# Kernel tuning notes

Hardware: AMD Instinct MI355X
Metric: run time of the kernel (lower is better)

## Reference

```python
import jax, jax.numpy as jnp
import numpy as np

DEPTH = 8
N_FEATURES = 512
N_CLASSES = 1000
N_LEAVES = 2 ** DEPTH          # 256
N_INTERNAL = N_LEAVES - 1      # 255
BATCH = 16384


def _path_tables():
    """Static routing tables for a complete binary tree (heap indexing).

    nodes[d, l] = internal node index visited at level d on the path to leaf l
    bits[d, l]  = 1 if path goes right at that node, else 0
    """
    leaves = np.arange(N_LEAVES)
    nodes = np.stack([(2 ** d - 1) + (leaves >> (DEPTH - d)) for d in range(DEPTH)])
    bits = np.stack([(leaves >> (DEPTH - 1 - d)) & 1 for d in range(DEPTH)])
    return nodes, bits


_NODES, _BITS = _path_tables()


def setup_inputs() -> dict:
    key = jax.random.key(0)
    k1, k2, k3 = jax.random.split(key, 3)
    x = jax.random.normal(k1, (BATCH, N_FEATURES), dtype=jnp.float32)
    # xavier-uniform-ish scale for the stacked gate weights
    gate_w = jax.random.normal(k2, (N_INTERNAL, N_FEATURES), dtype=jnp.float32) / np.sqrt(N_FEATURES)
    gate_b = jnp.zeros((N_INTERNAL,), dtype=jnp.float32)
    leaf_logits = jax.random.normal(k3, (N_LEAVES, N_CLASSES), dtype=jnp.float32) * 0.1
    return {"x": x, "gate_w": gate_w, "gate_b": gate_b, "leaf_logits": leaf_logits}


def reference(x, gate_w, gate_b, leaf_logits):
    # All internal-node gates as one batched matmul: [B, N_INTERNAL]
    p_right = jax.nn.sigmoid(jnp.einsum("bf,nf->bn", x, gate_w) + gate_b)
    # Arrival probability of each leaf: product of branch probs along its path.
    mu = jnp.ones((x.shape[0], N_LEAVES), dtype=x.dtype)
    for d in range(DEPTH):  # static loop over tree depth (8 iters)
        g = p_right[:, _NODES[d]]                       # [B, N_LEAVES]
        branch = jnp.where(_BITS[d] == 1, g, 1.0 - g)   # right vs left prob
        mu = mu * branch
    # Leaf class distributions: softmax per leaf over classes
    leaf_dists = jax.nn.softmax(leaf_logits, axis=-1)   # [N_LEAVES, N_CLASSES]
    return mu @ leaf_dists                              # [B, N_CLASSES]
```

## Files before the change

### kernel.cpp

```cpp
#include <hip/hip_runtime.h>

typedef __attribute__((ext_vector_type(8))) _Float16 f16x8;
typedef __attribute__((ext_vector_type(4))) _Float16 f16x4;
typedef __attribute__((ext_vector_type(4))) float   f32x4;

#define BATCH 16384
#define NFEAT 512
#define NCLS  1000
#define NLEAF 256
#define NINT  255
#define LDP   72
#define PSTR  257

__global__ __launch_bounds__(256) void prep(const float* __restrict__ L,
                                            _Float16* __restrict__ distF,
                                            const float* __restrict__ gw,
                                            _Float16* __restrict__ gwF) {
  const int t = threadIdx.x;
  const int wave = t >> 6, lane = t & 63;
  if (blockIdx.x >= 256) {
    const int p = (blockIdx.x - 256) * 4 + wave;
    const int c = (p >> 4) * 16 + (lane & 15);
    const int k0 = (p & 15) * 32 + (lane >> 4) * 8;
    f16x8 o = {};
    if (c < NINT) {
      float4 v0 = *(const float4*)&gw[(size_t)c * NFEAT + k0];
      float4 v1 = *(const float4*)&gw[(size_t)c * NFEAT + k0 + 4];
      o[0] = (_Float16)v0.x; o[1] = (_Float16)v0.y;
      o[2] = (_Float16)v0.z; o[3] = (_Float16)v0.w;
      o[4] = (_Float16)v1.x; o[5] = (_Float16)v1.y;
      o[6] = (_Float16)v1.z; o[7] = (_Float16)v1.w;
    }
    *(f16x8*)&gwF[((size_t)p * 64 + lane) * 8] = o;
    return;
  }
  __shared__ float red[4];
  const int l = blockIdx.x;
  const int kt = l >> 5, lhi_l = (l >> 3) & 3, jj = l & 7;
  float v[4];
  const bool live = t < 250;
  if (live) {
    float4 f = *(const float4*)&L[(size_t)l * NCLS + t * 4];
    v[0] = f.x; v[1] = f.y; v[2] = f.z; v[3] = f.w;
  } else {
    v[0] = v[1] = v[2] = v[3] = -1e30f;
  }
  float mx = fmaxf(fmaxf(v[0], v[1]), fmaxf(v[2], v[3]));
#pragma unroll
  for (int s = 32; s; s >>= 1) mx = fmaxf(mx, __shfl_xor(mx, s));
  if (lane == 0) red[wave] = mx;
  __syncthreads();
  mx = fmaxf(fmaxf(red[0], red[1]), fmaxf(red[2], red[3]));
  __syncthreads();
  float e[4], sum = 0.f;
#pragma unroll
  for (int i = 0; i < 4; ++i) { e[i] = __expf(v[i] - mx); sum += e[i]; }
  if (!live) { e[0] = e[1] = e[2] = e[3] = 0.f; sum = 0.f; }
#pragma unroll
  for (int s = 32; s; s >>= 1) sum += __shfl_xor(sum, s);
  if (lane == 0) red[wave] = sum;
  __syncthreads();
  sum = red[0] + red[1] + red[2] + red[3];
  float inv = 1.f / sum;
#pragma unroll
  for (int i = 0; i < 4; ++i) {
    int c = t * 4 + i;
    float val = live ? e[i] * inv : 0.f;
    int c16 = c >> 4, ln = c & 15;
    size_t idx = (((size_t)(c16 * 8 + kt)) * 64 + lhi_l * 16 + ln) * 8 + jj;
    distF[idx] = (_Float16)val;
  }
}

__global__ __launch_bounds__(1024)
void g1mu(const float* __restrict__ x, const _Float16* __restrict__ gwF,
          const float* __restrict__ gb, _Float16* __restrict__ muFg) {
  __shared__ union {
    _Float16 A[64 * LDP];
    float P[64 * PSTR];
  } sm;

  const int tid  = threadIdx.x;
  const int wave = tid >> 6, lane = tid & 63;
  const int ln15 = lane & 15, lhi = lane >> 4;
  const int r0 = blockIdx.x * 64;

  f32x4 acc1[4] = {};
  const int arow = tid >> 4, acol = (tid & 15) * 4;

  float4 pa = *(const float4*)&x[(size_t)(r0 + arow) * NFEAT + acol];
  for (int k = 0; k < NFEAT / 64; ++k) {
    {
      f16x4 h;
      h[0] = (_Float16)pa.x; h[1] = (_Float16)pa.y;
      h[2] = (_Float16)pa.z; h[3] = (_Float16)pa.w;
      *(f16x4*)&sm.A[arow * LDP + acol] = h;
    }
    __syncthreads();
    if (k < NFEAT / 64 - 1)
      pa = *(const float4*)&x[(size_t)(r0 + arow) * NFEAT + (k + 1) * 64 + acol];
#pragma unroll
    for (int kk = 0; kk < 2; ++kk) {
      f16x8 a[4];
#pragma unroll
      for (int m = 0; m < 4; ++m)
        a[m] = *(const f16x8*)&sm.A[(m * 16 + ln15) * LDP + kk * 32 + lhi * 8];
      f16x8 b = *(const f16x8*)&gwF[(((size_t)wave * 16 + k * 2 + kk) * 64 + lane) * 8];
#pragma unroll
      for (int m = 0; m < 4; ++m)
        acc1[m] = __builtin_amdgcn_mfma_f32_16x16x32_f16(a[m], b, acc1[m], 0, 0, 0);
    }
    __syncthreads();
  }

  {
    int col = wave * 16 + ln15;
    float bb = (col < NINT) ? gb[col] : 0.f;
#pragma unroll
    for (int m = 0; m < 4; ++m)
#pragma unroll
      for (int j = 0; j < 4; ++j) {
        int rl = m * 16 + lhi * 4 + j;
        float v = acc1[m][j] + bb;
        sm.P[rl * PSTR + col] = 1.f / (1.f + __expf(-v));
      }
  }
  __syncthreads();

  const int lf   = lane * 4;
  const int g_hi = lane >> 3;
  const int sub  = ((lane >> 1) & 3) * 16;
  const int j4   = (lane & 1) * 4;
#pragma unroll
  for (int rr = 0; rr < 4; ++rr) {
    int row = wave * 4 + rr;
    const float* p = &sm.P[row * PSTR];
    float pre = 1.f;
#pragma unroll
    for (int d = 0; d < 6; ++d) {
      int node = (1 << d) - 1 + (lf >> (8 - d));
      int bit  = (lf >> (7 - d)) & 1;
      float g = p[node];
      pre *= bit ? g : (1.f - g);
    }
    float g6  = p[63 + lane];
    float g7a = p[127 + 2 * lane];
    float g7b = p[128 + 2 * lane];
    f16x4 o;
    o[0] = (_Float16)(pre * (1.f - g6) * (1.f - g7a));
    o[1] = (_Float16)(pre * (1.f - g6) * g7a);
    o[2] = (_Float16)(pre * g6 * (1.f - g7b));
    o[3] = (_Float16)(pre * g6 * g7b);
    int row_g = r0 + row;
    size_t idx = (((size_t)(row_g >> 4) * 8 + g_hi) * 64 + sub + (row_g & 15)) * 8 + j4;
    *(f16x4*)&muFg[idx] = o;
  }
}

__global__ __launch_bounds__(256)
void g2(const _Float16* __restrict__ muFg, const _Float16* __restrict__ distF,
        float* __restrict__ out) {
  __shared__ _Float16 sMu[4 * 8 * 64 * 8];
  const int tid  = threadIdx.x;
  const int wave = tid >> 6, lane = tid & 63;
  const int ln15 = lane & 15, lhi = lane >> 4;
  const int bx = blockIdx.x;
  const int by = blockIdx.y;

  {
    const f16x8* src = (const f16x8*)(muFg + (size_t)bx * 16384);
    f16x8* dst = (f16x8*)sMu;
#pragma unroll
    for (int i = 0; i < 8; ++i)
      dst[tid + i * 256] = src[tid + i * 256];
  }
  __syncthreads();

  for (int h = 0; h < 4; ++h) {
    const int c16 = by * 16 + wave * 4 + h;
    f16x8 bb[8];
#pragma unroll
    for (int kk = 0; kk < 8; ++kk)
      bb[kk] = *(const f16x8*)&distF[(((size_t)c16 * 8 + kk) * 64 + lane) * 8];
#pragma unroll
    for (int g = 0; g < 4; ++g) {
      f32x4 acc = {};
#pragma unroll
      for (int kk = 0; kk < 8; ++kk) {
        f16x8 aa = *(const f16x8*)&sMu[((g * 8 + kk) * 64 + lane) * 8];
        acc = __builtin_amdgcn_mfma_f32_16x16x32_f16(bb[kk], aa, acc, 0, 0, 0);
      }
      const int brow = (bx * 4 + g) * 16 + ln15;
      const int col4 = c16 * 16 + lhi * 4;
      if (col4 < NCLS)
        *(f32x4*)&out[(size_t)brow * NCLS + col4] = acc;
    }
  }
}

extern "C" void kernel_launch(void* const* d_in, const int* in_sizes, int n_in,
                              void* d_out, int out_size, void* d_ws, size_t ws_size,
                              hipStream_t stream) {
  const float* x  = (const float*)d_in[0];
  const float* gw = (const float*)d_in[1];
  const float* gb = (const float*)d_in[2];
  const float* ll = (const float*)d_in[3];
  float* out = (float*)d_out;
  char* ws = (char*)d_ws;

  _Float16* gwF   = (_Float16*)(ws);
  _Float16* distF = (_Float16*)(ws + 262144);
  _Float16* muFg  = (_Float16*)(ws + 786432);

  prep <<<320, 256, 0, stream>>>(ll, distF, gw, gwF);
  g1mu <<<BATCH / 64, 1024, 0, stream>>>(x, gwF, gb, muFg);
  g2   <<<dim3(BATCH / 64, 4), 256, 0, stream>>>(muFg, distF, out);
}
```

Measured before the change: 53.79 us.

## Fuse gate/mu kernel with leaf-distribution GEMM, keeping mu in LDS

Merges the g1mu and g2 kernels into one 1024-thread kernel per 64-row block. The mu tile now stays in shared memory instead of going out to and back from a global workspace, and one kernel launch is removed. With 16 waves per block, each wave covers 4 column groups, so all 1000 classes are handled in one block instead of being split across 4 y-blocks. The cost is fewer blocks (256) doing the second GEMM and higher LDS use per block, which may reduce parallelism on the output phase.

New measurement: 101.5 us. 88.6% more time.

```diff
diff --git a/kernel.cpp b/kernel.cpp
--- a/kernel.cpp
+++ b/kernel.cpp
@@ -73,12 +73,14 @@
 }
 
 __global__ __launch_bounds__(1024)
-void g1mu(const float* __restrict__ x, const _Float16* __restrict__ gwF,
-          const float* __restrict__ gb, _Float16* __restrict__ muFg) {
+void fused(const float* __restrict__ x, const _Float16* __restrict__ gwF,
+           const float* __restrict__ gb, const _Float16* __restrict__ distF,
+           float* __restrict__ out) {
   __shared__ union {
     _Float16 A[64 * LDP];
     float P[64 * PSTR];
   } sm;
+  __shared__ _Float16 sMu[4 * 8 * 64 * 8];
 
   const int tid  = threadIdx.x;
   const int wave = tid >> 6, lane = tid & 63;
@@ -151,33 +153,13 @@
     o[1] = (_Float16)(pre * (1.f - g6) * g7a);
     o[2] = (_Float16)(pre * g6 * (1.f - g7b));
     o[3] = (_Float16)(pre * g6 * g7b);
-    int row_g = r0 + row;
-    size_t idx = (((size_t)(row_g >> 4) * 8 + g_hi) * 64 + sub + (row_g & 15)) * 8 + j4;
-    *(f16x4*)&muFg[idx] = o;
-  }
-}
-
-__global__ __launch_bounds__(256)
-void g2(const _Float16* __restrict__ muFg, const _Float16* __restrict__ distF,
-        float* __restrict__ out) {
-  __shared__ _Float16 sMu[4 * 8 * 64 * 8];
-  const int tid  = threadIdx.x;
-  const int wave = tid >> 6, lane = tid & 63;
-  const int ln15 = lane & 15, lhi = lane >> 4;
-  const int bx = blockIdx.x;
-  const int by = blockIdx.y;
-
-  {
-    const f16x8* src = (const f16x8*)(muFg + (size_t)bx * 16384);
-    f16x8* dst = (f16x8*)sMu;
-#pragma unroll
-    for (int i = 0; i < 8; ++i)
-      dst[tid + i * 256] = src[tid + i * 256];
+    size_t idx = (((size_t)(row >> 4) * 8 + g_hi) * 64 + sub + (row & 15)) * 8 + j4;
+    *(f16x4*)&sMu[idx] = o;
   }
   __syncthreads();
 
   for (int h = 0; h < 4; ++h) {
-    const int c16 = by * 16 + wave * 4 + h;
+    const int c16 = wave * 4 + h;
     f16x8 bb[8];
 #pragma unroll
     for (int kk = 0; kk < 8; ++kk)
@@ -190,7 +172,7 @@
         f16x8 aa = *(const f16x8*)&sMu[((g * 8 + kk) * 64 + lane) * 8];
         acc = __builtin_amdgcn_mfma_f32_16x16x32_f16(bb[kk], aa, acc, 0, 0, 0);
       }
-      const int brow = (bx * 4 + g) * 16 + ln15;
+      const int brow = r0 + g * 16 + ln15;
       const int col4 = c16 * 16 + lhi * 4;
       if (col4 < NCLS)
         *(f32x4*)&out[(size_t)brow * NCLS + col4] = acc;
@@ -210,9 +192,7 @@
 
   _Float16* gwF   = (_Float16*)(ws);
   _Float16* distF = (_Float16*)(ws + 262144);
-  _Float16* muFg  = (_Float16*)(ws + 786432);
 
-  prep <<<320, 256, 0, stream>>>(ll, distF, gw, gwF);
-  g1mu <<<BATCH / 64, 1024, 0, stream>>>(x, gwF, gb, muFg);
-  g2   <<<dim3(BATCH / 64, 4), 256, 0, stream>>>(muFg, distF, out);
+  prep  <<<320, 256, 0, stream>>>(ll, distF, gw, gwF);
+  fused <<<BATCH / 64, 1024, 0, stream>>>(x, gwF, gb, distF, out);
 }
```
